# Optimization experiments

Measured on AMD Instinct MI355X. Metric: run time of the kernel, lower is better.

## Reference

```python
import jax, jax.numpy as jnp
import numpy as np

B, S, D, H = 4, 2048, 1024, 16
DH = D // H  # per-head depth = 64
EPS = 1e-6


def setup_inputs() -> dict:
    key = jax.random.key(0)
    ks = jax.random.split(key, 12)
    sd = 1.0 / np.sqrt(D)
    return {
        "x": jax.random.normal(ks[0], (B, S, D), jnp.float32),
        "wq": jax.random.normal(ks[1], (D, D), jnp.float32) * sd,
        "bq": jnp.zeros((D,), jnp.float32),
        "wk": jax.random.normal(ks[2], (D, D), jnp.float32) * sd,
        "bk": jnp.zeros((D,), jnp.float32),
        "wv": jax.random.normal(ks[3], (D, D), jnp.float32) * sd,
        "bv": jnp.zeros((D,), jnp.float32),
        "wo": jax.random.normal(ks[4], (D, D), jnp.float32) * sd,
        "bo": jnp.zeros((D,), jnp.float32),
        "wf": jax.random.normal(ks[5], (D, D), jnp.float32) * sd,
        "bf": jnp.zeros((D,), jnp.float32),
        "g1": jnp.ones((D,), jnp.float32),
        "b1": jnp.zeros((D,), jnp.float32),
        "g2": jnp.ones((D,), jnp.float32),
        "b2": jnp.zeros((D,), jnp.float32),
    }


def _layernorm(x, gamma, beta):
    mu = jnp.mean(x, axis=-1, keepdims=True)
    var = jnp.mean(jnp.square(x - mu), axis=-1, keepdims=True)
    return (x - mu) * jax.lax.rsqrt(var + EPS) * gamma + beta


def reference(x, wq, bq, wk, bk, wv, bv, wo, bo, wf, bf, g1, b1, g2, b2):
    # --- multi-head attention (mask=None, is_resnet=False) ---
    def split_heads(t):  # [B,S,D] -> [B,H,S,DH]
        return t.reshape(B, S, H, DH).transpose(0, 2, 1, 3)

    q = split_heads(x @ wq + bq)
    k = split_heads(x @ wk + bk)
    v = split_heads(x @ wv + bv)

    scores = jnp.einsum("bhqd,bhkd->bhqk", q, k) / jnp.sqrt(
        jnp.asarray(DH, jnp.float32))
    attn = jax.nn.softmax(scores, axis=-1)
    ctx = jnp.einsum("bhqk,bhkd->bhqd", attn, v)  # [B,H,S,DH]
    ctx = ctx.transpose(0, 2, 1, 3).reshape(B, S, D)
    attn_out = ctx @ wo + bo

    # --- residual + LN, FFN (single Dense relu), residual + LN ---
    n1 = _layernorm(x + attn_out, g1, b1)
    fnn = jax.nn.relu(n1 @ wf + bf)
    n2 = _layernorm(fnn + n1, g2, b2)
    return n2
```

## Files before the change

### kernel.cpp

```cpp
#include <hip/hip_runtime.h>
#include <hip/hip_bf16.h>
#include <stdint.h>

using bf16 = __hip_bfloat16;
typedef float f32x4 __attribute__((ext_vector_type(4)));
typedef float f32x16 __attribute__((ext_vector_type(16)));
typedef short bf16x8 __attribute__((ext_vector_type(8)));
typedef uint32_t u32;

#define MFMA16(a, b, c) __builtin_amdgcn_mfma_f32_16x16x32_bf16(a, b, c, 0, 0, 0)
#define MFMA32(a, b, c) __builtin_amdgcn_mfma_f32_32x32x16_bf16(a, b, c, 0, 0, 0)

#define WAITVM(N) asm volatile("s_waitcnt vmcnt(" #N ")" ::: "memory")

__device__ __forceinline__ short f2bf(float f) {
  union { bf16 h; short s; } u;
  u.h = __float2bfloat16(f);
  return u.s;
}

__device__ __forceinline__ float b2f(short s) {
  union { u32 u; float f; } c;
  c.u = ((u32)(unsigned short)s) << 16;
  return c.f;
}

__device__ __forceinline__ float exp2fast(float x) {
#if __has_builtin(__builtin_amdgcn_exp2f)
  return __builtin_amdgcn_exp2f(x);
#else
  return exp2f(x);
#endif
}

__device__ __forceinline__ u32 cvt_pk_bf16(float lo, float hi) {
  u32 r;
  asm("v_cvt_pk_bf16_f32 %0, %1, %2" : "=v"(r) : "v"(lo), "v"(hi));
  return r;
}

#define ASYNC16(gp, lp)                                                        \
  __builtin_amdgcn_global_load_lds(                                            \
      (__attribute__((address_space(1))) void*)(uintptr_t)(const void*)(gp),   \
      (__attribute__((address_space(3))) void*)(uint32_t)(uintptr_t)(void*)(lp),\
      16, 0, 0)

__global__ __launch_bounds__(256) void wtrans5(
    const float* __restrict__ w0, const float* __restrict__ w1,
    const float* __restrict__ w2, const float* __restrict__ w3,
    const float* __restrict__ w4, bf16* __restrict__ wtbase) {
  __shared__ float t[64][65];
  const int z = blockIdx.z;
  const float* w = (z == 0) ? w0 : (z == 1) ? w1 : (z == 2) ? w2
                   : (z == 3) ? w3 : w4;
  bf16* wt = wtbase + (size_t)z * 1024 * 1024;
  const int nb = blockIdx.x * 64, kb = blockIdx.y * 64;
  const int tid = threadIdx.x;
  const int tx = tid & 63, ty = tid >> 6;
#pragma unroll
  for (int i = 0; i < 16; ++i)
    t[ty + i * 4][tx] = w[(size_t)(kb + ty + i * 4) * 1024 + nb + tx];
  __syncthreads();
#pragma unroll
  for (int i = 0; i < 16; ++i)
    wt[(size_t)(nb + ty + i * 4) * 1024 + kb + tx] =
        __float2bfloat16(t[tx][ty + i * 4]);
}

__global__ __launch_bounds__(256) void cvt4(const float* __restrict__ in,
                                            bf16* __restrict__ out) {
  const size_t i = (size_t)blockIdx.x * 256 + threadIdx.x;
  const float4 v = ((const float4*)in)[i];
  short4 o;
  o.x = f2bf(v.x); o.y = f2bf(v.y); o.z = f2bf(v.z); o.w = f2bf(v.w);
  ((short4*)out)[i] = o;
}

template <int EPI, int VT>
__global__ __launch_bounds__(512, 2) void gemm8(
    const bf16* __restrict__ A, const bf16* __restrict__ BT,
    const float* __restrict__ b0, const float* __restrict__ b1,
    const float* __restrict__ b2, const bf16* __restrict__ res,
    void* __restrict__ o0, void* __restrict__ o1, void* __restrict__ o2,
    float esc0) {
  constexpr int NT = 16;
  extern __shared__ char smem[];

  const int tid = threadIdx.x;
  const int lane = tid & 63, wid = tid >> 6;
  const int r = lane & 15, g = lane >> 4;
  const int r7 = r & 7;
  const int bm = blockIdx.x * 256, bn = blockIdx.y * 256;
  const int wm = (wid >> 2) * 128, wn = (wid & 3) * 64;

  const int rr3 = tid >> 3;
  const int gsw = (tid & 7) ^ (rr3 & 7);

  auto stageA = [&](int tile, int row0) {
    const bf16* src =
        A + (size_t)(bm + row0 + rr3) * 1024 + tile * 64 + gsw * 8;
    char* dst = smem + (tile & 1) * 32768 + (row0 + wid * 8) * 128;
    ASYNC16(src, dst);
  };
  auto stageB = [&](int tile, int row0) {
    const bf16* src =
        BT + (size_t)(bn + row0 + rr3) * 1024 + tile * 64 + gsw * 8;
    char* dst = smem + 65536 + (tile & 1) * 32768 + (row0 + wid * 8) * 128;
    ASYNC16(src, dst);
  };

  f32x4 acc[8][4] = {};

  stageB(0, 0); stageB(0, 128); stageB(0, 64); stageB(0, 192);
  stageA(0, 0); stageA(0, 128); stageA(0, 64); stageA(0, 192);
  stageB(1, 0); stageB(1, 128); stageB(1, 64); stageB(1, 192);

#define GPHASE(Q)                                                              \
  {                                                                            \
    if (Q == 0) { if (t + 1 < NT) { WAITVM(6); } else { WAITVM(2); } }         \
    if (Q == 2) { if (t + 1 < NT) { WAITVM(8); } else { WAITVM(0); } }         \
    __builtin_amdgcn_s_barrier();                                              \
    bf16x8 af[2][2];                                                           \
    _Pragma("unroll") for (int m2 = 0; m2 < 2; ++m2)                           \
      _Pragma("unroll") for (int s = 0; s < 2; ++s)                            \
        af[m2][s] = *(const bf16x8*)(Ab + (2 * Q + m2) * 2048 +                \
                                     (((4 * s + g) ^ r7) << 4));               \
    if (Q == 0) {                                                              \
      _Pragma("unroll") for (int nf = 0; nf < 4; ++nf)                         \
        _Pragma("unroll") for (int s = 0; s < 2; ++s)                          \
          bfr[nf][s] = *(const bf16x8*)(Bb + nf * 2048 +                       \
                                        (((4 * s + g) ^ r7) << 4));            \
    }                                                                          \
    if (Q == 0 && t + 1 < NT) { stageA(t + 1, 0); stageA(t + 1, 128); }        \
    if (Q == 1 && t + 1 < NT) { stageA(t + 1, 64); stageA(t + 1, 192); }       \
    if (Q == 2 && t + 2 < NT) { stageB(t + 2, 0); stageB(t + 2, 128); }        \
    if (Q == 3 && t + 2 < NT) { stageB(t + 2, 64); stageB(t + 2, 192); }       \
    __builtin_amdgcn_s_setprio(1);                                             \
    _Pragma("unroll") for (int m2 = 0; m2 < 2; ++m2)                           \
      _Pragma("unroll") for (int nf = 0; nf < 4; ++nf) {                       \
        acc[2 * Q + m2][nf] = MFMA16(af[m2][0], bfr[nf][0], acc[2*Q+m2][nf]);  \
        acc[2 * Q + m2][nf] = MFMA16(af[m2][1], bfr[nf][1], acc[2*Q+m2][nf]);  \
      }                                                                        \
    __builtin_amdgcn_s_setprio(0);                                             \
  }

  for (int t = 0; t < NT; ++t) {
    const int buf = t & 1;
    const char* Ab = smem + buf * 32768 + (wm + r) * 128;
    const char* Bb = smem + 65536 + buf * 32768 + (wn + r) * 128;
    bf16x8 bfr[4][2];
    GPHASE(0)
    GPHASE(1)
    GPHASE(2)
    GPHASE(3)
  }
#undef GPHASE

  const int seg = blockIdx.y >> 2;
  const float* bias = (seg == 0) ? b0 : (seg == 1) ? b1 : b2;
  void* outp = (seg == 0) ? o0 : (seg == 1) ? o1 : o2;
  const float esc = (seg == 0) ? esc0 : 1.f;
  const int colbase = (bn & 1023) + wn;
#pragma unroll
  for (int mf = 0; mf < 8; ++mf) {
    if (EPI == 0 && VT && seg == 2) {
      const int row0 = bm + wm + mf * 16 + g * 4;
#pragma unroll
      for (int nf = 0; nf < 4; ++nf) {
        const int col = colbase + nf * 16 + r;
        const float bvv = bias[col];
        short4 o;
        o.x = f2bf(acc[mf][nf][0] + bvv);
        o.y = f2bf(acc[mf][nf][1] + bvv);
        o.z = f2bf(acc[mf][nf][2] + bvv);
        o.w = f2bf(acc[mf][nf][3] + bvv);
        const size_t idx =
            (((size_t)(row0 >> 11) * 16 + (col >> 6)) * 64 + (col & 63)) *
                2048 + (row0 & 2047);
        *(short4*)((bf16*)o2 + idx) = o;
      }
    } else {
#pragma unroll
      for (int rr = 0; rr < 4; ++rr) {
        const size_t row = (size_t)bm + wm + mf * 16 + g * 4 + rr;
#pragma unroll
        for (int nf = 0; nf < 4; ++nf) {
          const int col = colbase + nf * 16 + r;
          float v = acc[mf][nf][rr] + bias[col];
          if (EPI == 0) {
            ((bf16*)outp)[row * 1024 + col] = __float2bfloat16(v * esc);
          } else if (EPI == 1) {
            ((bf16*)outp)[row * 1024 + col] = __float2bfloat16(
                v + b2f(((const short*)res)[row * 1024 + col]));
          } else {
            ((bf16*)outp)[row * 1024 + col] = __float2bfloat16(
                fmaxf(v, 0.f) + b2f(((const short*)res)[row * 1024 + col]));
          }
        }
      }
    }
  }
}

__global__ __launch_bounds__(256, 3) void attn32(const bf16* __restrict__ Q,
                                                 const bf16* __restrict__ K,
                                                 const bf16* __restrict__ Vt,
                                                 bf16* __restrict__ ctx) {
  constexpr int S = 2048, D = 1024;
  __shared__ alignas(16) bf16 sK[2][64][64];
  __shared__ alignas(16) bf16 sV[2][64][64];

  const int id = blockIdx.x;
  const int xcd = id & 7, kk = id >> 3;
  const int bh = xcd * 8 + (kk & 7), qb = kk >> 3;
  const int b = bh >> 4, h = bh & 15;
  const int tid = threadIdx.x;
  const int lane = tid & 63, w = tid >> 6;
  const int lq = lane & 31, hi = lane >> 5;
  const int r7 = lq & 7;

  const bf16* qp = Q + ((size_t)(b * S + qb * 128 + w * 32 + lq)) * D +
                   h * 64 + hi * 8;
  bf16x8 qf[4];
#pragma unroll
  for (int ch = 0; ch < 4; ++ch) qf[ch] = *(const bf16x8*)(qp + ch * 16);

  f32x16 oacc[2] = {};
  float l = 0.f;

  const bf16* kg = K + (size_t)b * S * D + h * 64;
  const bf16* vg = Vt + (size_t)bh * 64 * S;
  const int srow = lane >> 3;
  const int sg = (lane & 7) ^ srow;

  auto stage = [&](int kt, int buf) {
    const int kv0 = kt * 64;
#pragma unroll
    for (int i = 0; i < 2; ++i) {
      const int c = 2 * w + i;
      const int row = c * 8 + srow;
      ASYNC16(kg + (size_t)(kv0 + row) * D + sg * 8, &sK[buf][c * 8][0]);
      ASYNC16(vg + (size_t)row * S + kv0 + sg * 8, &sV[buf][c * 8][0]);
    }
  };

  stage(0, 0);
  for (int kt = 0; kt < S / 64; ++kt) {
    __syncthreads();
    if (kt + 1 < S / 64) stage(kt + 1, (kt + 1) & 1);
    const int buf = kt & 1;

    const char* kb = (const char*)&sK[buf][0][0] + (size_t)lq * 128;
    f32x16 s0 = {}, s1 = {};
#pragma unroll
    for (int ch = 0; ch < 4; ++ch) {
      const int gb = ((ch * 2 + hi) ^ r7) * 16;
      const bf16x8 k0 = *(const bf16x8*)(kb + gb);
      const bf16x8 k1 = *(const bf16x8*)(kb + 32 * 128 + gb);
      s0 = MFMA32(k0, qf[ch], s0);
      s1 = MFMA32(k1, qf[ch], s1);
    }

    u32 pk[2][8];
    float ps = 0.f;
#pragma unroll
    for (int u = 0; u < 8; ++u) {
      const float p0 = exp2fast(s0[2 * u]);
      const float p1 = exp2fast(s0[2 * u + 1]);
      const float p2 = exp2fast(s1[2 * u]);
      const float p3 = exp2fast(s1[2 * u + 1]);
      ps += (p0 + p1) + (p2 + p3);
      pk[0][u] = cvt_pk_bf16(p0, p1);
      pk[1][u] = cvt_pk_bf16(p2, p3);
    }
    l += ps;

    const char* vb = (const char*)&sV[buf][0][0] + (size_t)lq * 128;
#pragma unroll
    for (int ch = 0; ch < 4; ++ch) {
      const int t = ch >> 1, M = (ch & 1) * 4;
      u32 a0 = pk[t][M + 0], a1 = pk[t][M + 1];
      u32 a2 = pk[t][M + 2], a3 = pk[t][M + 3];
      asm("v_permlane32_swap_b32 %0, %1" : "+v"(a0), "+v"(a2));
      asm("v_permlane32_swap_b32 %0, %1" : "+v"(a1), "+v"(a3));
      union { u32 u4[4]; bf16x8 v; } fr;
      fr.u4[0] = a0; fr.u4[1] = a1; fr.u4[2] = a2; fr.u4[3] = a3;
      const int gb = ((ch * 2 + hi) ^ r7) * 16;
      const bf16x8 v0 = *(const bf16x8*)(vb + gb);
      const bf16x8 v1 = *(const bf16x8*)(vb + 32 * 128 + gb);
      oacc[0] = MFMA32(fr.v, v0, oacc[0]);
      oacc[1] = MFMA32(fr.v, v1, oacc[1]);
    }
  }

  l += __shfl_xor(l, 32);
  const float linv = 1.f / l;
  const size_t obase =
      ((size_t)(b * S + qb * 128 + w * 32)) * D + h * 64 + lq;
#pragma unroll
  for (int reg = 0; reg < 16; ++reg) {
    const int qr = (reg & 3) + 8 * (reg >> 2) + 4 * hi;
    const float li = __shfl(linv, qr);
    ctx[obase + (size_t)qr * D] = __float2bfloat16(oacc[0][reg] * li);
    ctx[obase + (size_t)qr * D + 32] = __float2bfloat16(oacc[1][reg] * li);
  }
}

template <int OUTF>
__global__ __launch_bounds__(256) void ln_bf(const bf16* __restrict__ in,
                                             const float* __restrict__ gam,
                                             const float* __restrict__ bet,
                                             float* __restrict__ outf,
                                             bf16* __restrict__ outb) {
  const int row = blockIdx.x, tid = threadIdx.x;
  const short4 sv = ((const short4*)in)[(size_t)row * 256 + tid];
  float4 v;
  v.x = b2f(sv.x); v.y = b2f(sv.y); v.z = b2f(sv.z); v.w = b2f(sv.w);
  float s = v.x + v.y + v.z + v.w;
  float s2 = v.x * v.x + v.y * v.y + v.z * v.z + v.w * v.w;
  const int lane = tid & 63, w = tid >> 6;
#pragma unroll
  for (int mk = 1; mk < 64; mk <<= 1) {
    s += __shfl_xor(s, mk);
    s2 += __shfl_xor(s2, mk);
  }
  __shared__ float red[8];
  if (lane == 0) { red[w] = s; red[4 + w] = s2; }
  __syncthreads();
  s = red[0] + red[1] + red[2] + red[3];
  s2 = red[4] + red[5] + red[6] + red[7];
  const float mu = s * (1.f / 1024.f);
  const float var = s2 * (1.f / 1024.f) - mu * mu;
  const float rstd = rsqrtf(var + 1e-6f);
  const float4 gv = ((const float4*)gam)[tid];
  const float4 bv = ((const float4*)bet)[tid];
  float4 o;
  o.x = (v.x - mu) * rstd * gv.x + bv.x;
  o.y = (v.y - mu) * rstd * gv.y + bv.y;
  o.z = (v.z - mu) * rstd * gv.z + bv.z;
  o.w = (v.w - mu) * rstd * gv.w + bv.w;
  if (OUTF) {
    ((float4*)(outf + (size_t)row * 1024))[tid] = o;
  } else {
    short4 ob;
    ob.x = f2bf(o.x); ob.y = f2bf(o.y); ob.z = f2bf(o.z); ob.w = f2bf(o.w);
    ((short4*)outb)[(size_t)row * 256 + tid] = ob;
  }
}

extern "C" void kernel_launch(void* const* d_in, const int* in_sizes, int n_in,
                              void* d_out, int out_size, void* d_ws,
                              size_t ws_size, hipStream_t stream) {
  const float* x   = (const float*)d_in[0];
  const float* wq  = (const float*)d_in[1];
  const float* bq  = (const float*)d_in[2];
  const float* wk  = (const float*)d_in[3];
  const float* bk  = (const float*)d_in[4];
  const float* wv  = (const float*)d_in[5];
  const float* bv  = (const float*)d_in[6];
  const float* wo  = (const float*)d_in[7];
  const float* bo  = (const float*)d_in[8];
  const float* wf  = (const float*)d_in[9];
  const float* bfb = (const float*)d_in[10];
  const float* g1  = (const float*)d_in[11];
  const float* b1  = (const float*)d_in[12];
  const float* g2  = (const float*)d_in[13];
  const float* b2  = (const float*)d_in[14];
  float* out = (float*)d_out;

  char* ws = (char*)d_ws;
  const size_t MB = 1ull << 20;
  bf16* wtq = (bf16*)(ws + 0 * MB);
  bf16* wto = (bf16*)(ws + 6 * MB);
  bf16* wtf = (bf16*)(ws + 8 * MB);
  bf16* xbf = (bf16*)(ws + 10 * MB);
  bf16* qbf = (bf16*)(ws + 26 * MB);
  bf16* kbf = (bf16*)(ws + 42 * MB);
  bf16* vt  = (bf16*)(ws + 74 * MB);
  bf16* ctx = (bf16*)(ws + 90 * MB);
  bf16* y   = (bf16*)(ws + 26 * MB);
  bf16* n1b = (bf16*)(ws + 42 * MB);
  bf16* hb  = (bf16*)(ws + 58 * MB);

  const float qsc = 0.125f * 1.44269504f;

  const dim3 b256(256);
  wtrans5<<<dim3(16, 16, 5), b256, 0, stream>>>(wq, wk, wv, wo, wf, wtq);
  cvt4<<<dim3(8192), b256, 0, stream>>>(x, xbf);

  gemm8<0, 1><<<dim3(32, 12), dim3(512), 131072, stream>>>(
      xbf, wtq, bq, bk, bv, nullptr, qbf, kbf, vt, qsc);

  attn32<<<dim3(1024), b256, 0, stream>>>(qbf, kbf, vt, ctx);

  gemm8<1, 0><<<dim3(32, 4), dim3(512), 131072, stream>>>(
      ctx, wto, bo, bo, bo, xbf, y, y, y, 1.f);
  ln_bf<0><<<dim3(8192), b256, 0, stream>>>(y, g1, b1, nullptr, n1b);
  gemm8<2, 0><<<dim3(32, 4), dim3(512), 131072, stream>>>(
      n1b, wtf, bfb, bfb, bfb, n1b, hb, hb, hb, 1.f);
  ln_bf<1><<<dim3(8192), b256, 0, stream>>>(hb, g2, b2, out, nullptr);
}
```

Baseline: 232.3 us.

## Halve GEMM M-tile to 128 rows to double grid size

The GEMM kernel now uses a 128x256 block tile instead of 256x256. Each wave computes 64x64, with matching changes to the staging schedule, wait counts and shared-memory layout (96KB instead of 128KB). This doubles the number of blocks so the out-projection and FFN GEMMs (128 blocks before) can fill more of the CUs, and lower LDS use may allow more resident blocks. The cost is less data reuse per tile: B is reloaded for twice as many blocks, and there are fewer MFMAs per barrier.

```diff
diff --git a/kernel.cpp b/kernel.cpp
--- a/kernel.cpp
+++ b/kernel.cpp
@@ -77,7 +77,7 @@
 }
 
 template <int EPI, int VT>
-__global__ __launch_bounds__(512, 2) void gemm8(
+__global__ __launch_bounds__(512, 2) void gemmh(
     const bf16* __restrict__ A, const bf16* __restrict__ BT,
     const float* __restrict__ b0, const float* __restrict__ b1,
     const float* __restrict__ b2, const bf16* __restrict__ res,
@@ -90,8 +90,8 @@
   const int lane = tid & 63, wid = tid >> 6;
   const int r = lane & 15, g = lane >> 4;
   const int r7 = r & 7;
-  const int bm = blockIdx.x * 256, bn = blockIdx.y * 256;
-  const int wm = (wid >> 2) * 128, wn = (wid & 3) * 64;
+  const int bm = blockIdx.x * 128, bn = blockIdx.y * 256;
+  const int wm = (wid >> 2) * 64, wn = (wid & 3) * 64;
 
   const int rr3 = tid >> 3;
   const int gsw = (tid & 7) ^ (rr3 & 7);
@@ -99,62 +99,58 @@
   auto stageA = [&](int tile, int row0) {
     const bf16* src =
         A + (size_t)(bm + row0 + rr3) * 1024 + tile * 64 + gsw * 8;
-    char* dst = smem + (tile & 1) * 32768 + (row0 + wid * 8) * 128;
+    char* dst = smem + (tile & 1) * 16384 + (row0 + wid * 8) * 128;
     ASYNC16(src, dst);
   };
   auto stageB = [&](int tile, int row0) {
     const bf16* src =
         BT + (size_t)(bn + row0 + rr3) * 1024 + tile * 64 + gsw * 8;
-    char* dst = smem + 65536 + (tile & 1) * 32768 + (row0 + wid * 8) * 128;
+    char* dst = smem + 32768 + (tile & 1) * 32768 + (row0 + wid * 8) * 128;
     ASYNC16(src, dst);
   };
 
-  f32x4 acc[8][4] = {};
-
-  stageB(0, 0); stageB(0, 128); stageB(0, 64); stageB(0, 192);
-  stageA(0, 0); stageA(0, 128); stageA(0, 64); stageA(0, 192);
-  stageB(1, 0); stageB(1, 128); stageB(1, 64); stageB(1, 192);
-
-#define GPHASE(Q)                                                              \
+  f32x4 acc[4][4] = {};
+
+  stageB(0, 0); stageB(0, 64); stageB(0, 128); stageB(0, 192);
+  stageA(0, 0); stageA(0, 64);
+  stageB(1, 0); stageB(1, 64); stageB(1, 128); stageB(1, 192);
+
+#define HPHASE(Q)                                                              \
   {                                                                            \
-    if (Q == 0) { if (t + 1 < NT) { WAITVM(6); } else { WAITVM(2); } }         \
-    if (Q == 2) { if (t + 1 < NT) { WAITVM(8); } else { WAITVM(0); } }         \
+    if (Q == 0) { if (t + 1 < NT) { WAITVM(4); } else { WAITVM(0); } }         \
+    if (Q == 2) { if (t + 1 < NT) { WAITVM(6); } }                             \
     __builtin_amdgcn_s_barrier();                                              \
-    bf16x8 af[2][2];                                                           \
-    _Pragma("unroll") for (int m2 = 0; m2 < 2; ++m2)                           \
-      _Pragma("unroll") for (int s = 0; s < 2; ++s)                            \
-        af[m2][s] = *(const bf16x8*)(Ab + (2 * Q + m2) * 2048 +                \
-                                     (((4 * s + g) ^ r7) << 4));               \
+    bf16x8 af[2];                                                              \
+    _Pragma("unroll") for (int s = 0; s < 2; ++s)                              \
+      af[s] = *(const bf16x8*)(Ab + Q * 2048 + (((4 * s + g) ^ r7) << 4));     \
     if (Q == 0) {                                                              \
       _Pragma("unroll") for (int nf = 0; nf < 4; ++nf)                         \
         _Pragma("unroll") for (int s = 0; s < 2; ++s)                          \
           bfr[nf][s] = *(const bf16x8*)(Bb + nf * 2048 +                       \
                                         (((4 * s + g) ^ r7) << 4));            \
     }                                                                          \
-    if (Q == 0 && t + 1 < NT) { stageA(t + 1, 0); stageA(t + 1, 128); }        \
-    if (Q == 1 && t + 1 < NT) { stageA(t + 1, 64); stageA(t + 1, 192); }       \
+    if (Q == 0 && t + 1 < NT) { stageA(t + 1, 0); stageA(t + 1, 64); }         \
     if (Q == 2 && t + 2 < NT) { stageB(t + 2, 0); stageB(t + 2, 128); }        \
     if (Q == 3 && t + 2 < NT) { stageB(t + 2, 64); stageB(t + 2, 192); }       \
     __builtin_amdgcn_s_setprio(1);                                             \
-    _Pragma("unroll") for (int m2 = 0; m2 < 2; ++m2)                           \
-      _Pragma("unroll") for (int nf = 0; nf < 4; ++nf) {                       \
-        acc[2 * Q + m2][nf] = MFMA16(af[m2][0], bfr[nf][0], acc[2*Q+m2][nf]);  \
-        acc[2 * Q + m2][nf] = MFMA16(af[m2][1], bfr[nf][1], acc[2*Q+m2][nf]);  \
-      }                                                                        \
+    _Pragma("unroll") for (int nf = 0; nf < 4; ++nf) {                         \
+      acc[Q][nf] = MFMA16(af[0], bfr[nf][0], acc[Q][nf]);                      \
+      acc[Q][nf] = MFMA16(af[1], bfr[nf][1], acc[Q][nf]);                      \
+    }                                                                          \
     __builtin_amdgcn_s_setprio(0);                                             \
   }
 
   for (int t = 0; t < NT; ++t) {
     const int buf = t & 1;
-    const char* Ab = smem + buf * 32768 + (wm + r) * 128;
-    const char* Bb = smem + 65536 + buf * 32768 + (wn + r) * 128;
+    const char* Ab = smem + buf * 16384 + (wm + r) * 128;
+    const char* Bb = smem + 32768 + buf * 32768 + (wn + r) * 128;
     bf16x8 bfr[4][2];
-    GPHASE(0)
-    GPHASE(1)
-    GPHASE(2)
-    GPHASE(3)
-  }
-#undef GPHASE
+    HPHASE(0)
+    HPHASE(1)
+    HPHASE(2)
+    HPHASE(3)
+  }
+#undef HPHASE
 
   const int seg = blockIdx.y >> 2;
   const float* bias = (seg == 0) ? b0 : (seg == 1) ? b1 : b2;
@@ -162,7 +158,7 @@
   const float esc = (seg == 0) ? esc0 : 1.f;
   const int colbase = (bn & 1023) + wn;
 #pragma unroll
-  for (int mf = 0; mf < 8; ++mf) {
+  for (int mf = 0; mf < 4; ++mf) {
     if (EPI == 0 && VT && seg == 2) {
       const int row0 = bm + wm + mf * 16 + g * 4;
 #pragma unroll
@@ -388,15 +384,15 @@
   wtrans5<<<dim3(16, 16, 5), b256, 0, stream>>>(wq, wk, wv, wo, wf, wtq);
   cvt4<<<dim3(8192), b256, 0, stream>>>(x, xbf);
 
-  gemm8<0, 1><<<dim3(32, 12), dim3(512), 131072, stream>>>(
+  gemmh<0, 1><<<dim3(64, 12), dim3(512), 98304, stream>>>(
       xbf, wtq, bq, bk, bv, nullptr, qbf, kbf, vt, qsc);
 
   attn32<<<dim3(1024), b256, 0, stream>>>(qbf, kbf, vt, ctx);
 
-  gemm8<1, 0><<<dim3(32, 4), dim3(512), 131072, stream>>>(
+  gemmh<1, 0><<<dim3(64, 4), dim3(512), 98304, stream>>>(
       ctx, wto, bo, bo, bo, xbf, y, y, y, 1.f);
   ln_bf<0><<<dim3(8192), b256, 0, stream>>>(y, g1, b1, nullptr, n1b);
-  gemm8<2, 0><<<dim3(32, 4), dim3(512), 131072, stream>>>(
+  gemmh<2, 0><<<dim3(64, 4), dim3(512), 98304, stream>>>(
       n1b, wtf, bfb, bfb, bfb, n1b, hb, hb, hb, 1.f);
   ln_bf<1><<<dim3(8192), b256, 0, stream>>>(hb, g2, b2, out, nullptr);
 }
```

Result: faster. 204.5 us (-12.0%).
